# Optimization experiments

Hardware: AMD Instinct MI355X
Metric: run time of the kernel (lower is better)

Reference implementation:

```python
import jax, jax.numpy as jnp
import numpy as np

N_NODES = 100000
N_EDGES = 1600000
D_IN = 128
D_MSG = 128
D_HID = 128
D_EDGE = 5
D_CAT = D_IN + D_MSG  # 256
D_U1, D_U2, D_OUT = 214, 172, 128  # delta = (256-128)//3 = 42


def _leaky(x):
    return jax.nn.leaky_relu(x, negative_slope=0.01)


def setup_inputs() -> dict:
    key = jax.random.key(0)
    ks = jax.random.split(key, 12)
    def kaiming(k, shape):
        fan_in = shape[1]
        gain = np.sqrt(2.0 / (1.0 + 0.01 ** 2))
        return jax.random.normal(k, shape, dtype=jnp.float32) * (gain / np.sqrt(fan_in))
    x = jax.random.normal(ks[0], (N_NODES, D_IN), dtype=jnp.float32)
    edge_index = jax.random.randint(ks[1], (2, N_EDGES), 0, N_NODES, dtype=jnp.int64)
    edge_attr = jax.random.normal(ks[2], (N_EDGES, D_EDGE), dtype=jnp.float32)
    return {
        "x": x, "edge_index": edge_index, "edge_attr": edge_attr,
        "Wm1": kaiming(ks[3], (D_HID, D_EDGE)), "bm1": jnp.zeros((D_HID,), jnp.float32),
        "Wm2": kaiming(ks[4], (D_HID, D_HID)), "bm2": jnp.zeros((D_HID,), jnp.float32),
        "Wm3": kaiming(ks[5], (D_MSG, D_HID)), "bm3": jnp.zeros((D_MSG,), jnp.float32),
        "ln_g": jnp.ones((D_CAT,), jnp.float32), "ln_b": jnp.zeros((D_CAT,), jnp.float32),
        "Wu1": kaiming(ks[6], (D_U1, D_CAT)), "bu1": jnp.zeros((D_U1,), jnp.float32),
        "Wu2": kaiming(ks[7], (D_U2, D_U1)), "bu2": jnp.zeros((D_U2,), jnp.float32),
        "Wu3": kaiming(ks[8], (D_OUT, D_U2)), "bu3": jnp.zeros((D_OUT,), jnp.float32),
    }


def reference(x, edge_index, edge_attr, Wm1, bm1, Wm2, bm2, Wm3, bm3,
              ln_g, ln_b, Wu1, bu1, Wu2, bu2, Wu3, bu3):
    # --- message: MLP2 on edge_attr only ---  [E, D_MSG]
    h = _leaky(edge_attr @ Wm1.T + bm1)
    h = _leaky(h @ Wm2.T + bm2)
    msg = h @ Wm3.T + bm3
    # --- aggregate: scatter-add per destination node (edge_index[1]) ---
    dst = edge_index[1]
    aggr = jax.ops.segment_sum(msg, dst, num_segments=x.shape[0])  # [N, D_MSG]
    # --- update: LayerNorm(concat) then shrinking MLP ---
    cat = jnp.concatenate([x, aggr], axis=-1)  # [N, 256]
    mu = jnp.mean(cat, axis=-1, keepdims=True)
    var = jnp.mean((cat - mu) ** 2, axis=-1, keepdims=True)
    nrm = (cat - mu) * jax.lax.rsqrt(var + 1e-5) * ln_g + ln_b
    u = _leaky(nrm @ Wu1.T + bu1)
    u = _leaky(u @ Wu2.T + bu2)
    return u @ Wu3.T + bu3  # [N, D_OUT]
```

## Files before the change

### kernel.cpp

```cpp
#include <hip/hip_runtime.h>

#define N_NODES 100000
#define N_EDGES 1600000
#define STRN 264
#define NBLK_SCAN 391

#define MSG_SCALE 4096.0f
#define MSG_INV   0.000244140625f

typedef __attribute__((ext_vector_type(4))) float floatx4;
typedef __attribute__((ext_vector_type(8))) __bf16 bf16x8;
typedef __attribute__((ext_vector_type(8))) unsigned short ushort8;
typedef __attribute__((ext_vector_type(4))) unsigned short ushort4v;

#define WS_AGGR   0ull
#define WS_COUNTS 51200000ull
#define WS_OFFS   51600384ull
#define WS_PART   52000768ull
#define WS_DSTS   52002816ull
#define WS_ATTRS  58402816ull
#define WS_W2     90402816ull
#define WS_W3     (WS_W2 + 32768ull)
#define WS_WU1    (WS_W3 + 32768ull)
#define WS_WU2    (WS_WU1 + 114688ull)
#define WS_WU3    (WS_WU2 + 86016ull)
#define WS_W1     (WS_WU3 + 49152ull)

__device__ __forceinline__ unsigned short tobf(float f) {
  return __builtin_bit_cast(unsigned short, (__bf16)f);
}

__device__ __forceinline__ float leaky(float v) { return fmaxf(v, 0.01f * v); }

__device__ __forceinline__ int swz(int row, int ch) {
  return row * 128 + (ch ^ ((row & 7) << 3));
}

__global__ void prep_kernel(const float* __restrict__ Wm1, const float* __restrict__ Wm2,
                            const float* __restrict__ Wm3,
                            const float* __restrict__ Wu1, const float* __restrict__ Wu2,
                            const float* __restrict__ Wu3,
                            unsigned short* __restrict__ o1b,
                            unsigned short* __restrict__ o2, unsigned short* __restrict__ o3,
                            unsigned short* __restrict__ o1p, unsigned short* __restrict__ o2p,
                            unsigned short* __restrict__ o3p) {
  int i = blockIdx.x * 256 + threadIdx.x;
  if (i < 16384) {
    o2[i] = tobf(Wm2[i]);
  } else if (i < 32768) {
    int j = i - 16384; o3[j] = tobf(Wm3[j]);
  } else if (i < 32768 + 57344) {
    int j = i - 32768; int n = j >> 8, k = j & 255;
    o1p[j] = (n < 214) ? tobf(Wu1[n * 256 + k]) : (unsigned short)0;
  } else if (i < 90112 + 43008) {
    int j = i - 90112; int n = j / 224, k = j - n * 224;
    o2p[j] = (n < 172 && k < 214) ? tobf(Wu2[n * 214 + k]) : (unsigned short)0;
  } else if (i < 133120 + 24576) {
    int j = i - 133120; int n = j / 192, k = j - n * 192;
    o3p[j] = (k < 172) ? tobf(Wu3[n * 172 + k]) : (unsigned short)0;
  } else if (i < 157696 + 4096) {
    int j = i - 157696; int n = j >> 5, k = j & 31;
    o1b[j] = (k < 5) ? tobf(Wm1[n * 5 + k]) : (unsigned short)0;
  }
}

__global__ void hist_kernel(const int* __restrict__ dst, int* __restrict__ counts,
                            int* __restrict__ rank) {
  int e = blockIdx.x * 256 + threadIdx.x;
  if (e < N_EDGES) rank[e] = atomicAdd(&counts[dst[e]], 1);
}

__global__ void scanA_kernel(const int* __restrict__ counts, int* __restrict__ offs,
                             int* __restrict__ partials) {
  __shared__ int tmp[256];
  const int t = threadIdx.x;
  const int i = blockIdx.x * 256 + t;
  int v = (i < N_NODES) ? counts[i] : 0;
  tmp[t] = v;
  __syncthreads();
  for (int off = 1; off < 256; off <<= 1) {
    int a = (t >= off) ? tmp[t - off] : 0;
    __syncthreads();
    tmp[t] += a;
    __syncthreads();
  }
  if (i < N_NODES) offs[i] = tmp[t] - v;
  if (t == 255) partials[blockIdx.x] = tmp[255];
}

__global__ void scanB_kernel(int* __restrict__ partials) {
  __shared__ int tmp[512];
  const int t = threadIdx.x;
  int v = (t < NBLK_SCAN) ? partials[t] : 0;
  tmp[t] = v;
  __syncthreads();
  for (int off = 1; off < 512; off <<= 1) {
    int a = (t >= off) ? tmp[t - off] : 0;
    __syncthreads();
    tmp[t] += a;
    __syncthreads();
  }
  if (t < NBLK_SCAN) partials[t] = tmp[t] - v;
}

__global__ void scatter_kernel(const int* __restrict__ dst, const int* __restrict__ offs,
                               const int* __restrict__ parts, const int* __restrict__ rank,
                               const float* __restrict__ attr,
                               unsigned short* __restrict__ attrB, int* __restrict__ dsts) {
  int e = blockIdx.x * 256 + threadIdx.x;
  if (e < N_EDGES) {
    int d = dst[e];
    int p = offs[d] + parts[d >> 8] + rank[e];
    dsts[p] = d;
    const float* a = attr + (size_t)e * 5;
    ushort8 v;
    v[0] = tobf(a[0]); v[1] = tobf(a[1]); v[2] = tobf(a[2]);
    v[3] = tobf(a[3]); v[4] = tobf(a[4]);
    v[5] = 0; v[6] = 0; v[7] = 0;
    *(ushort8*)(void*)&attrB[(size_t)p * 8] = v;
  }
}

__global__ __launch_bounds__(256, 4) void edge_kernel(
    const unsigned short* __restrict__ attrB, const int* __restrict__ dsts,
    const unsigned short* __restrict__ W1bf, const float* __restrict__ bm1,
    const unsigned short* __restrict__ W2bf, const float* __restrict__ bm2,
    const unsigned short* __restrict__ W3bf, const float* __restrict__ bm3,
    int* __restrict__ aggr) {
  __shared__ __align__(16) char smem[33280];
  unsigned short* sH = (unsigned short*)(void*)smem;
  unsigned short* sAttrB = sH;
  int* sMsgI = (int*)(void*)smem;
  int* sDst = (int*)(void*)(smem + 32768);

  const int t = threadIdx.x;
  const int wave = t >> 6, lane = t & 63;
  const int col = lane & 15, q = lane >> 4;
  const int wbase = wave * 32;
  const long blockEdge = (long)blockIdx.x * 128;

  if (t < 128) {
    *(ushort8*)(void*)&sAttrB[t * 40] =
        *(const ushort8*)(const void*)&attrB[(blockEdge + t) * 8];
    sDst[t] = dsts[blockEdge + t];
  }
  {
    ushort8 z;
#pragma unroll
    for (int j = 0; j < 8; j++) z[j] = 0;
#pragma unroll
    for (int i = 0; i < 2; i++) {
      const int idx = i * 256 + t;
      const int row = idx >> 2, part = idx & 3;
      *(ushort8*)(void*)&sAttrB[row * 40 + 8 + part * 8] = z;
    }
  }
  __syncthreads();

  floatx4 acc[2][8];

  {
    bf16x8 w1f[2];
#pragma unroll
    for (int i = 0; i < 2; i++)
      w1f[i] = *(const bf16x8*)(const void*)&W1bf[(wbase + i * 16 + col) * 32 + q * 8];
#pragma unroll
    for (int i = 0; i < 2; i++)
#pragma unroll
      for (int j = 0; j < 8; j++) acc[i][j] = (floatx4){0.f, 0.f, 0.f, 0.f};
#pragma unroll
    for (int et = 0; et < 8; et++) {
      bf16x8 b = *(const bf16x8*)(const void*)&sAttrB[(et * 16 + col) * 40 + q * 8];
      acc[0][et] = __builtin_amdgcn_mfma_f32_16x16x32_bf16(w1f[0], b, acc[0][et], 0, 0, 0);
      acc[1][et] = __builtin_amdgcn_mfma_f32_16x16x32_bf16(w1f[1], b, acc[1][et], 0, 0, 0);
    }
  }
  __syncthreads();

  {
    float4 blo = *(const float4*)&bm1[wbase + q * 4];
    float4 bhi = *(const float4*)&bm1[wbase + 16 + q * 4];
#pragma unroll
    for (int et = 0; et < 8; et++) {
      const int e = et * 16 + col;
      ushort4v plo, phi;
#pragma unroll
      for (int r = 0; r < 4; r++) {
        plo[r] = tobf(leaky(acc[0][et][r] + ((const float*)&blo)[r]));
        phi[r] = tobf(leaky(acc[1][et][r] + ((const float*)&bhi)[r]));
      }
      *(ushort4v*)(void*)&sH[swz(e, wbase + q * 4)] = plo;
      *(ushort4v*)(void*)&sH[swz(e, wbase + 16 + q * 4)] = phi;
    }
  }
  __syncthreads();

  {
    bf16x8 w2f[2][4];
#pragma unroll
    for (int i = 0; i < 2; i++)
#pragma unroll
      for (int ks = 0; ks < 4; ks++)
        w2f[i][ks] = *(const bf16x8*)(const void*)
            &W2bf[(wbase + i * 16 + col) * 128 + ks * 32 + q * 8];
#pragma unroll
    for (int i = 0; i < 2; i++)
#pragma unroll
      for (int j = 0; j < 8; j++) acc[i][j] = (floatx4){0.f, 0.f, 0.f, 0.f};
#pragma unroll
    for (int ks = 0; ks < 4; ks++) {
      const int kk = ks * 32 + q * 8;
#pragma unroll
      for (int et = 0; et < 8; et++) {
        bf16x8 hb = *(const bf16x8*)(const void*)&sH[swz(et * 16 + col, kk)];
        acc[0][et] = __builtin_amdgcn_mfma_f32_16x16x32_bf16(w2f[0][ks], hb, acc[0][et], 0, 0, 0);
        acc[1][et] = __builtin_amdgcn_mfma_f32_16x16x32_bf16(w2f[1][ks], hb, acc[1][et], 0, 0, 0);
      }
    }
  }
  __syncthreads();

  {
    float4 blo = *(const float4*)&bm2[wbase + q * 4];
    float4 bhi = *(const float4*)&bm2[wbase + 16 + q * 4];
#pragma unroll
    for (int et = 0; et < 8; et++) {
      const int e = et * 16 + col;
      ushort4v plo, phi;
#pragma unroll
      for (int r = 0; r < 4; r++) {
        plo[r] = tobf(leaky(acc[0][et][r] + ((const float*)&blo)[r]));
        phi[r] = tobf(leaky(acc[1][et][r] + ((const float*)&bhi)[r]));
      }
      *(ushort4v*)(void*)&sH[swz(e, wbase + q * 4)] = plo;
      *(ushort4v*)(void*)&sH[swz(e, wbase + 16 + q * 4)] = phi;
    }
  }
  __syncthreads();

  {
    bf16x8 w3f[2][4];
#pragma unroll
    for (int i = 0; i < 2; i++)
#pragma unroll
      for (int ks = 0; ks < 4; ks++)
        w3f[i][ks] = *(const bf16x8*)(const void*)
            &W3bf[(wbase + i * 16 + col) * 128 + ks * 32 + q * 8];
#pragma unroll
    for (int i = 0; i < 2; i++)
#pragma unroll
      for (int j = 0; j < 8; j++) acc[i][j] = (floatx4){0.f, 0.f, 0.f, 0.f};
#pragma unroll
    for (int ks = 0; ks < 4; ks++) {
      const int kk = ks * 32 + q * 8;
#pragma unroll
      for (int et = 0; et < 8; et++) {
        bf16x8 hb = *(const bf16x8*)(const void*)&sH[swz(et * 16 + col, kk)];
        acc[0][et] = __builtin_amdgcn_mfma_f32_16x16x32_bf16(w3f[0][ks], hb, acc[0][et], 0, 0, 0);
        acc[1][et] = __builtin_amdgcn_mfma_f32_16x16x32_bf16(w3f[1][ks], hb, acc[1][et], 0, 0, 0);
      }
    }
  }
  __syncthreads();

  const int dmy = sDst[wave * 32 + (lane & 31)];

#pragma unroll
  for (int c = 0; c < 2; c++) {
    if ((wave >> 1) == c) {
#pragma unroll
      for (int ci = 0; ci < 2; ci++) {
        float4 b3 = *(const float4*)&bm3[wbase + ci * 16 + q * 4];
        const int cb = (wbase + ci * 16 + q * 4) & 63;
#pragma unroll
        for (int et = 0; et < 8; et++) {
          const int e = et * 16 + col;
          int4 p;
          p.x = __float2int_rn((acc[ci][et][0] + b3.x) * MSG_SCALE);
          p.y = __float2int_rn((acc[ci][et][1] + b3.y) * MSG_SCALE);
          p.z = __float2int_rn((acc[ci][et][2] + b3.z) * MSG_SCALE);
          p.w = __float2int_rn((acc[ci][et][3] + b3.w) * MSG_SCALE);
          *(int4*)(void*)&sMsgI[e * 64 + (cb ^ ((e & 7) << 2))] = p;
        }
      }
    }
    __syncthreads();

    const int e0 = wave * 32;
    const size_t chG = (size_t)c * 64 + lane;
    int accv = 0;
    int dprev = __builtin_amdgcn_readlane(dmy, 0);
#pragma unroll 8
    for (int it = 0; it < 32; it++) {
      const int e = e0 + it;
      const int d = __builtin_amdgcn_readlane(dmy, it);
      const int iv = sMsgI[e * 64 + (lane ^ ((e & 7) << 2))];
      if (d != dprev) {
        atomicAdd(&aggr[(size_t)dprev * 128 + chG], accv);
        accv = 0;
        dprev = d;
      }
      accv += iv;
    }
    atomicAdd(&aggr[(size_t)dprev * 128 + chG], accv);
    if (c == 0) __syncthreads();
  }
}

template <int TILES, int CT, int KST, bool FINAL>
__device__ __forceinline__ void layer_node_sw(unsigned short* __restrict__ sX,
                                              const unsigned short* __restrict__ W,
                                              const float* __restrict__ bias, int biasLim,
                                              int wave, int lane, int nodeGBase,
                                              float* __restrict__ out) {
  const int col = lane & 15, q = lane >> 4;
  const int K = KST * 32;
  floatx4 acc[CT][4];
#pragma unroll
  for (int c = 0; c < CT; c++)
#pragma unroll
    for (int n = 0; n < 4; n++) acc[c][n] = (floatx4){0.f, 0.f, 0.f, 0.f};

#pragma unroll
  for (int ks = 0; ks < KST; ks++) {
    const int kk = ks * 32 + q * 8;
    bf16x8 a[CT];
#pragma unroll
    for (int c = 0; c < CT; c++) {
      const int tile = wave + 4 * c;
      const int tc = (tile < TILES) ? tile : 0;
      a[c] = *(const bf16x8*)(const void*)&W[(tc * 16 + col) * K + kk];
    }
    bf16x8 b[4];
#pragma unroll
    for (int n = 0; n < 4; n++)
      b[n] = *(const bf16x8*)(const void*)&sX[(n * 16 + col) * STRN + kk];
#pragma unroll
    for (int c = 0; c < CT; c++) {
      if (wave + 4 * c < TILES) {
#pragma unroll
        for (int n = 0; n < 4; n++)
          acc[c][n] = __builtin_amdgcn_mfma_f32_16x16x32_bf16(a[c], b[n], acc[c][n], 0, 0, 0);
      }
    }
  }
  __syncthreads();

#pragma unroll
  for (int c = 0; c < CT; c++) {
    const int tile = wave + 4 * c;
    if (tile < TILES) {
      float bv[4];
#pragma unroll
      for (int r = 0; r < 4; r++) {
        const int ch = tile * 16 + q * 4 + r;
        bv[r] = (ch < biasLim) ? bias[ch] : 0.f;
      }
#pragma unroll
      for (int n = 0; n < 4; n++) {
        const int node = n * 16 + col;
        if (!FINAL) {
          ushort4v p;
#pragma unroll
          for (int r = 0; r < 4; r++) p[r] = tobf(leaky(acc[c][n][r] + bv[r]));
          *(ushort4v*)(void*)&sX[node * STRN + tile * 16 + q * 4] = p;
        } else {
          const long ng = (long)nodeGBase + node;
          if (ng < N_NODES) {
            float4 p = make_float4(acc[c][n][0] + bv[0], acc[c][n][1] + bv[1],
                                   acc[c][n][2] + bv[2], acc[c][n][3] + bv[3]);
            *(float4*)(void*)&out[ng * 128 + tile * 16 + q * 4] = p;
          }
        }
      }
    }
  }
  if (!FINAL) __syncthreads();
}

__global__ __launch_bounds__(256, 4) void node_kernel(
    const float* __restrict__ x, const int* __restrict__ aggr,
    const float* __restrict__ lng, const float* __restrict__ lnb,
    const unsigned short* __restrict__ Wu1p, const float* __restrict__ bu1,
    const unsigned short* __restrict__ Wu2p, const float* __restrict__ bu2,
    const unsigned short* __restrict__ Wu3p, const float* __restrict__ bu3,
    float* __restrict__ out) {
  __shared__ unsigned short sX[64 * STRN];
  __shared__ float sG[256], sB[256];
  const int t = threadIdx.x;
  const int wave = t >> 6, lane = t & 63;
  sG[t] = lng[t];
  sB[t] = lnb[t];

  const int nl = t >> 2;
  const int part = t & 3;
  const long nodeG = (long)blockIdx.x * 64 + nl;
  const bool valid = nodeG < N_NODES;
  const float* srcF = x + nodeG * 128 + part * 64;
  const int* srcI = aggr + nodeG * 128 + (part - 2) * 64;
  float s = 0.f, ss = 0.f;
  if (valid) {
#pragma unroll
    for (int i = 0; i < 16; i++) {
      float4 a;
      if (part < 2) {
        a = *(const float4*)(srcF + i * 4);
      } else {
        int4 iv = *(const int4*)(srcI + i * 4);
        a = make_float4(iv.x * MSG_INV, iv.y * MSG_INV, iv.z * MSG_INV, iv.w * MSG_INV);
      }
      s += a.x + a.y + a.z + a.w;
      ss += a.x * a.x + a.y * a.y + a.z * a.z + a.w * a.w;
    }
  }
  s += __shfl_xor(s, 1); s += __shfl_xor(s, 2);
  ss += __shfl_xor(ss, 1); ss += __shfl_xor(ss, 2);
  const float mean = s * (1.f / 256.f);
  const float var = ss * (1.f / 256.f) - mean * mean;
  const float rstd = rsqrtf(var + 1e-5f);
  __syncthreads();
  if (valid) {
    const int cb = part * 64;
#pragma unroll
    for (int i = 0; i < 16; i++) {
      float4 a;
      if (part < 2) {
        a = *(const float4*)(srcF + i * 4);
      } else {
        int4 iv = *(const int4*)(srcI + i * 4);
        a = make_float4(iv.x * MSG_INV, iv.y * MSG_INV, iv.z * MSG_INV, iv.w * MSG_INV);
      }
      int c = cb + i * 4;
      ushort4v p;
      p[0] = tobf((a.x - mean) * rstd * sG[c + 0] + sB[c + 0]);
      p[1] = tobf((a.y - mean) * rstd * sG[c + 1] + sB[c + 1]);
      p[2] = tobf((a.z - mean) * rstd * sG[c + 2] + sB[c + 2]);
      p[3] = tobf((a.w - mean) * rstd * sG[c + 3] + sB[c + 3]);
      *(ushort4v*)(void*)&sX[nl * STRN + c] = p;
    }
  }
  __syncthreads();

  const int nodeGBase = blockIdx.x * 64;
  layer_node_sw<14, 4, 8, false>(sX, Wu1p, bu1, 214, wave, lane, nodeGBase, nullptr);
  layer_node_sw<12, 3, 7, false>(sX, Wu2p, bu2, 172, wave, lane, nodeGBase, nullptr);
  layer_node_sw<8, 2, 6, true>(sX, Wu3p, bu3, 128, wave, lane, nodeGBase, out);
}

extern "C" void kernel_launch(void* const* d_in, const int* in_sizes, int n_in,
                              void* d_out, int out_size, void* d_ws, size_t ws_size,
                              hipStream_t stream) {
  const float* x    = (const float*)d_in[0];
  const int*   eidx = (const int*)d_in[1];
  const float* attr = (const float*)d_in[2];
  const float* Wm1  = (const float*)d_in[3];
  const float* bm1  = (const float*)d_in[4];
  const float* Wm2  = (const float*)d_in[5];
  const float* bm2  = (const float*)d_in[6];
  const float* Wm3  = (const float*)d_in[7];
  const float* bm3  = (const float*)d_in[8];
  const float* lng  = (const float*)d_in[9];
  const float* lnb  = (const float*)d_in[10];
  const float* Wu1  = (const float*)d_in[11];
  const float* bu1  = (const float*)d_in[12];
  const float* Wu2  = (const float*)d_in[13];
  const float* bu2  = (const float*)d_in[14];
  const float* Wu3  = (const float*)d_in[15];
  const float* bu3  = (const float*)d_in[16];
  float* out = (float*)d_out;

  char* ws = (char*)d_ws;
  int* aggr    = (int*)(ws + WS_AGGR);
  int* rank    = (int*)(ws + WS_AGGR);
  int* counts  = (int*)(ws + WS_COUNTS);
  int* offs    = (int*)(ws + WS_OFFS);
  int* parts   = (int*)(ws + WS_PART);
  int* dsts    = (int*)(ws + WS_DSTS);
  unsigned short* attrB = (unsigned short*)(ws + WS_ATTRS);
  unsigned short* W2bf = (unsigned short*)(ws + WS_W2);
  unsigned short* W3bf = (unsigned short*)(ws + WS_W3);
  unsigned short* Wu1p = (unsigned short*)(ws + WS_WU1);
  unsigned short* Wu2p = (unsigned short*)(ws + WS_WU2);
  unsigned short* Wu3p = (unsigned short*)(ws + WS_WU3);
  unsigned short* W1bf = (unsigned short*)(ws + WS_W1);

  const int* dst = eidx + N_EDGES;

  hipMemsetAsync(counts, 0, 400384, stream);
  hist_kernel<<<6250, 256, 0, stream>>>(dst, counts, rank);
  scanA_kernel<<<NBLK_SCAN, 256, 0, stream>>>(counts, offs, parts);
  scanB_kernel<<<1, 512, 0, stream>>>(parts);
  scatter_kernel<<<6250, 256, 0, stream>>>(dst, offs, parts, rank, attr, attrB, dsts);

  hipMemsetAsync(aggr, 0, (size_t)N_NODES * 128 * sizeof(int), stream);
  prep_kernel<<<632, 256, 0, stream>>>(Wm1, Wm2, Wm3, Wu1, Wu2, Wu3,
                                       W1bf, W2bf, W3bf, Wu1p, Wu2p, Wu3p);

  edge_kernel<<<N_EDGES / 128, 256, 0, stream>>>(attrB, dsts, W1bf, bm1, W2bf, bm2, W3bf,
                                                 bm3, aggr);
  node_kernel<<<(N_NODES + 63) / 64, 256, 0, stream>>>(x, aggr, lng, lnb, Wu1p, bu1, Wu2p, bu2,
                                                       Wu3p, bu3, out);
}
```

Baseline: 594.1 us.

## Fuse histogram with weight prep, pack dst into attr slots, zero aggr in scatter

Merges the weight-conversion prep kernel into the histogram kernel and removes the separate dsts array by packing each edge's destination index into the unused padding of its bf16 attribute record. The aggregation buffer memset is replaced by zeroing inside the scatter kernel, which works because each of the 1.6M edge threads clears 8 ints, covering 100000*128 ints exactly. The rank array moves to its own workspace region so that zeroing aggr in scatter does not overwrite ranks that are still being read. The intent is to cut two launches plus a memset and one index stream, at the cost of more coupled kernels and a zeroing step that depends on the edge count matching the node buffer size.

New measurement: 578.4 us. -2.6%, faster.

```diff
diff --git a/kernel.cpp b/kernel.cpp
--- a/kernel.cpp
+++ b/kernel.cpp
@@ -17,7 +17,7 @@
 #define WS_COUNTS 51200000ull
 #define WS_OFFS   51600384ull
 #define WS_PART   52000768ull
-#define WS_DSTS   52002816ull
+#define WS_RANK   52002816ull
 #define WS_ATTRS  58402816ull
 #define WS_W2     90402816ull
 #define WS_W3     (WS_W2 + 32768ull)
@@ -36,15 +36,18 @@
   return row * 128 + (ch ^ ((row & 7) << 3));
 }
 
-__global__ void prep_kernel(const float* __restrict__ Wm1, const float* __restrict__ Wm2,
-                            const float* __restrict__ Wm3,
-                            const float* __restrict__ Wu1, const float* __restrict__ Wu2,
-                            const float* __restrict__ Wu3,
-                            unsigned short* __restrict__ o1b,
-                            unsigned short* __restrict__ o2, unsigned short* __restrict__ o3,
-                            unsigned short* __restrict__ o1p, unsigned short* __restrict__ o2p,
-                            unsigned short* __restrict__ o3p) {
+__global__ void hist_prep_kernel(const int* __restrict__ dst, int* __restrict__ counts,
+                                 int* __restrict__ rank,
+                                 const float* __restrict__ Wm1, const float* __restrict__ Wm2,
+                                 const float* __restrict__ Wm3,
+                                 const float* __restrict__ Wu1, const float* __restrict__ Wu2,
+                                 const float* __restrict__ Wu3,
+                                 unsigned short* __restrict__ o1b,
+                                 unsigned short* __restrict__ o2, unsigned short* __restrict__ o3,
+                                 unsigned short* __restrict__ o1p, unsigned short* __restrict__ o2p,
+                                 unsigned short* __restrict__ o3p) {
   int i = blockIdx.x * 256 + threadIdx.x;
+  if (i < N_EDGES) rank[i] = atomicAdd(&counts[dst[i]], 1);
   if (i < 16384) {
     o2[i] = tobf(Wm2[i]);
   } else if (i < 32768) {
@@ -64,12 +67,6 @@
   }
 }
 
-__global__ void hist_kernel(const int* __restrict__ dst, int* __restrict__ counts,
-                            int* __restrict__ rank) {
-  int e = blockIdx.x * 256 + threadIdx.x;
-  if (e < N_EDGES) rank[e] = atomicAdd(&counts[dst[e]], 1);
-}
-
 __global__ void scanA_kernel(const int* __restrict__ counts, int* __restrict__ offs,
                              int* __restrict__ partials) {
   __shared__ int tmp[256];
@@ -106,23 +103,28 @@
 __global__ void scatter_kernel(const int* __restrict__ dst, const int* __restrict__ offs,
                                const int* __restrict__ parts, const int* __restrict__ rank,
                                const float* __restrict__ attr,
-                               unsigned short* __restrict__ attrB, int* __restrict__ dsts) {
+                               unsigned short* __restrict__ attrB, int* __restrict__ aggr) {
   int e = blockIdx.x * 256 + threadIdx.x;
   if (e < N_EDGES) {
     int d = dst[e];
     int p = offs[d] + parts[d >> 8] + rank[e];
-    dsts[p] = d;
     const float* a = attr + (size_t)e * 5;
     ushort8 v;
     v[0] = tobf(a[0]); v[1] = tobf(a[1]); v[2] = tobf(a[2]);
     v[3] = tobf(a[3]); v[4] = tobf(a[4]);
-    v[5] = 0; v[6] = 0; v[7] = 0;
+    v[5] = 0;
+    v[6] = (unsigned short)(d & 0xffff);
+    v[7] = (unsigned short)(d >> 16);
     *(ushort8*)(void*)&attrB[(size_t)p * 8] = v;
+    int4 z = make_int4(0, 0, 0, 0);
+    int4* ag = (int4*)(void*)&aggr[(size_t)e * 8];
+    ag[0] = z;
+    ag[1] = z;
   }
 }
 
 __global__ __launch_bounds__(256, 4) void edge_kernel(
-    const unsigned short* __restrict__ attrB, const int* __restrict__ dsts,
+    const unsigned short* __restrict__ attrB,
     const unsigned short* __restrict__ W1bf, const float* __restrict__ bm1,
     const unsigned short* __restrict__ W2bf, const float* __restrict__ bm2,
     const unsigned short* __restrict__ W3bf, const float* __restrict__ bm3,
@@ -140,9 +142,10 @@
   const long blockEdge = (long)blockIdx.x * 128;
 
   if (t < 128) {
-    *(ushort8*)(void*)&sAttrB[t * 40] =
-        *(const ushort8*)(const void*)&attrB[(blockEdge + t) * 8];
-    sDst[t] = dsts[blockEdge + t];
+    ushort8 v = *(const ushort8*)(const void*)&attrB[(blockEdge + t) * 8];
+    sDst[t] = (int)v[6] | ((int)v[7] << 16);
+    v[6] = 0; v[7] = 0;
+    *(ushort8*)(void*)&sAttrB[t * 40] = v;
   }
   {
     ushort8 z;
@@ -471,11 +474,10 @@
 
   char* ws = (char*)d_ws;
   int* aggr    = (int*)(ws + WS_AGGR);
-  int* rank    = (int*)(ws + WS_AGGR);
   int* counts  = (int*)(ws + WS_COUNTS);
   int* offs    = (int*)(ws + WS_OFFS);
   int* parts   = (int*)(ws + WS_PART);
-  int* dsts    = (int*)(ws + WS_DSTS);
+  int* rank    = (int*)(ws + WS_RANK);
   unsigned short* attrB = (unsigned short*)(ws + WS_ATTRS);
   unsigned short* W2bf = (unsigned short*)(ws + WS_W2);
   unsigned short* W3bf = (unsigned short*)(ws + WS_W3);
@@ -487,16 +489,14 @@
   const int* dst = eidx + N_EDGES;
 
   hipMemsetAsync(counts, 0, 400384, stream);
-  hist_kernel<<<6250, 256, 0, stream>>>(dst, counts, rank);
+  hist_prep_kernel<<<6250, 256, 0, stream>>>(dst, counts, rank,
+                                             Wm1, Wm2, Wm3, Wu1, Wu2, Wu3,
+                                             W1bf, W2bf, W3bf, Wu1p, Wu2p, Wu3p);
   scanA_kernel<<<NBLK_SCAN, 256, 0, stream>>>(counts, offs, parts);
   scanB_kernel<<<1, 512, 0, stream>>>(parts);
-  scatter_kernel<<<6250, 256, 0, stream>>>(dst, offs, parts, rank, attr, attrB, dsts);
-
-  hipMemsetAsync(aggr, 0, (size_t)N_NODES * 128 * sizeof(int), stream);
-  prep_kernel<<<632, 256, 0, stream>>>(Wm1, Wm2, Wm3, Wu1, Wu2, Wu3,
-                                       W1bf, W2bf, W3bf, Wu1p, Wu2p, Wu3p);
-
-  edge_kernel<<<N_EDGES / 128, 256, 0, stream>>>(attrB, dsts, W1bf, bm1, W2bf, bm2, W3bf,
+  scatter_kernel<<<6250, 256, 0, stream>>>(dst, offs, parts, rank, attr, attrB, aggr);
+
+  edge_kernel<<<N_EDGES / 128, 256, 0, stream>>>(attrB, W1bf, bm1, W2bf, bm2, W3bf,
                                                  bm3, aggr);
   node_kernel<<<(N_NODES + 63) / 64, 256, 0, stream>>>(x, aggr, lng, lnb, Wu1p, bu1, Wu2p, bu2,
                                                        Wu3p, bu3, out);
```
